# Performance work log

Hardware: AMD Instinct MI355X
Metric: run time of the kernel (lower is better)

## Reference

```python
import jax, jax.numpy as jnp
import numpy as np

B, N, D, H = 16, 256, 1024, 8
DK = D // H
WAVE_LEN = 1000.0


def box_relational_embedding(boxes):
    # boxes: (B, N, 4) as (x_min, y_min, x_max, y_max)
    x_min, y_min, x_max, y_max = jnp.split(boxes, 4, axis=-1)  # each (B, N, 1)
    cx = (x_min + x_max) * 0.5
    cy = (y_min + y_max) * 0.5
    w = (x_max - x_min) + 1.0
    h = (y_max - y_min) + 1.0
    # pairwise deltas (B, N, N); row i = query box, col j = key box
    delta_x = jnp.log(jnp.clip(jnp.abs((cx - jnp.swapaxes(cx, -2, -1)) / w), 1e-3, None))
    delta_y = jnp.log(jnp.clip(jnp.abs((cy - jnp.swapaxes(cy, -2, -1)) / h), 1e-3, None))
    delta_w = jnp.log(w / jnp.swapaxes(w, -2, -1))
    delta_h = jnp.log(h / jnp.swapaxes(h, -2, -1))
    pos = jnp.stack([delta_x, delta_y, delta_w, delta_h], axis=-1)  # (B, N, N, 4)
    # sinusoidal expansion: dim_g = 64 -> 8 frequencies per delta
    feat_range = jnp.arange(8, dtype=pos.dtype) / 8.0
    dim_mat = 1.0 / (WAVE_LEN ** feat_range)  # (8,)
    mul = (100.0 * pos)[..., None] * dim_mat  # (B, N, N, 4, 8)
    mul = mul.reshape(pos.shape[:3] + (32,))
    return jnp.concatenate([jnp.sin(mul), jnp.cos(mul)], axis=-1)  # (B, N, N, 64)


def setup_inputs() -> dict:
    key = jax.random.key(0)
    ks = jax.random.split(key, 12)
    x = jax.random.normal(ks[0], (B, N, D), dtype=jnp.float32)
    # valid boxes: x_max > x_min, y_max > y_min
    xy = jax.random.uniform(ks[1], (B, N, 2), dtype=jnp.float32) * 100.0
    wh = jax.random.uniform(ks[2], (B, N, 2), dtype=jnp.float32) * 50.0 + 1.0
    boxes = jnp.concatenate([xy, xy + wh], axis=-1)
    s = 1.0 / np.sqrt(D)
    Wq = jax.random.normal(ks[3], (D, D), dtype=jnp.float32) * s
    Wk = jax.random.normal(ks[4], (D, D), dtype=jnp.float32) * s
    Wv = jax.random.normal(ks[5], (D, D), dtype=jnp.float32) * s
    Wo = jax.random.normal(ks[6], (D, D), dtype=jnp.float32) * s
    bq = jnp.zeros((D,), jnp.float32)
    bk = jnp.zeros((D,), jnp.float32)
    bv = jnp.zeros((D,), jnp.float32)
    bo = jnp.zeros((D,), jnp.float32)
    Wg = jax.random.normal(ks[7], (H, 64), dtype=jnp.float32) * (1.0 / 8.0)  # 8 per-head (64->1) linears
    bg = jnp.zeros((H,), jnp.float32)
    return {"x": x, "boxes": boxes, "Wq": Wq, "bq": bq, "Wk": Wk, "bk": bk,
            "Wv": Wv, "bv": bv, "Wo": Wo, "bo": bo, "Wg": Wg, "bg": bg}


def reference(x, boxes, Wq, bq, Wk, bk, Wv, bv, Wo, bo, Wg, bg):
    emb = box_relational_embedding(boxes)  # (B, N, N, 64)
    # per-head geometric weights, ReLU'd: (B, H, N, N)
    geo = jax.nn.relu(jnp.einsum('bnmg,hg->bhnm', emb, Wg) + bg[None, :, None, None])
    q = (x @ Wq + bq).reshape(B, N, H, DK).transpose(0, 2, 1, 3)  # (B, H, N, DK)
    k = (x @ Wk + bk).reshape(B, N, H, DK).transpose(0, 2, 1, 3)
    v = (x @ Wv + bv).reshape(B, N, H, DK).transpose(0, 2, 1, 3)
    scores = jnp.einsum('bhnd,bhmd->bhnm', q, k) / np.sqrt(DK)
    w_mn = jax.nn.softmax(jnp.log(jnp.clip(geo, 1e-6, None)) + scores, axis=-1)
    out = jnp.einsum('bhnm,bhmd->bhnd', w_mn, v)  # (B, H, N, DK)
    out = out.transpose(0, 2, 1, 3).reshape(B, N, D)
    return out @ Wo + bo
```

## Files before the change

### kernel.cpp

```cpp
#include <hip/hip_runtime.h>
#include <hip/hip_fp16.h>

#define Bb 16
#define Nn 256
#define Dd 1024
#define Hh 8
#define DKk 128

typedef unsigned short u16;
typedef __attribute__((ext_vector_type(8))) short bfrag;
typedef __attribute__((ext_vector_type(4))) float f4;

#define MFMA16(a, b, c) __builtin_amdgcn_mfma_f32_16x16x32_bf16((a), (b), (c), 0, 0, 0)

__device__ __forceinline__ u16 f2b(float f) {
  unsigned int u = __builtin_bit_cast(unsigned int, f);
  u += 0x7fffu + ((u >> 16) & 1u);
  return (u16)(u >> 16);
}

typedef __attribute__((address_space(1))) void GV;
typedef __attribute__((address_space(3))) void LV;
__device__ __forceinline__ void gload16(const void* g, void* l) {
  __builtin_amdgcn_global_load_lds((GV*)g, (LV*)l, 16, 0, 0);
}

__global__ __launch_bounds__(256) void cast_x_kernel(const float* __restrict__ x,
                                                     u16* __restrict__ xb) {
  const int i = blockIdx.x * 256 + threadIdx.x;
  const float4 v = ((const float4*)x)[i];
  union { u16 u[4]; unsigned long long ll; } p;
  p.u[0] = f2b(v.x); p.u[1] = f2b(v.y); p.u[2] = f2b(v.z); p.u[3] = f2b(v.w);
  ((unsigned long long*)xb)[i] = p.ll;
}

__global__ __launch_bounds__(256) void transpose_w_kernel(
    const float* __restrict__ Wq, const float* __restrict__ Wk,
    const float* __restrict__ Wv, const float* __restrict__ Wo,
    u16* __restrict__ wqkvt, u16* __restrict__ wot) {
  __shared__ float t[32][33];
  const int bid = blockIdx.x;
  const int which = bid >> 10;
  const int tr = (bid >> 5) & 31;
  const int tc = bid & 31;
  const float* W = which == 0 ? Wq : which == 1 ? Wk : which == 2 ? Wv : Wo;
  u16* dst = (which == 3) ? wot : (wqkvt + (long long)which * 1024 * 1024);
  const int tx = threadIdx.x & 31, ty = threadIdx.x >> 5;
#pragma unroll
  for (int rr = 0; rr < 4; rr++)
    t[ty + rr * 8][tx] = W[(tr * 32 + ty + rr * 8) * 1024 + tc * 32 + tx];
  __syncthreads();
#pragma unroll
  for (int rr = 0; rr < 4; rr++)
    dst[(tc * 32 + ty + rr * 8) * 1024 + tr * 32 + tx] = f2b(t[tx][ty + rr * 8]);
}

__global__ __launch_bounds__(256) void transpose_v_kernel(const u16* __restrict__ v,
                                                          u16* __restrict__ vT) {
  __shared__ u16 t[32][33];
  const int bid = blockIdx.x;
  const int bh = bid >> 5;
  const int kt = (bid >> 2) & 7;
  const int ct = bid & 3;
  const u16* src = v + (long long)bh * Nn * DKk;
  u16* dst = vT + (long long)bh * DKk * Nn;
  const int tx = threadIdx.x & 31, ty = threadIdx.x >> 5;
#pragma unroll
  for (int rr = 0; rr < 4; rr++)
    t[ty + rr * 8][tx] = src[(kt * 32 + ty + rr * 8) * DKk + ct * 32 + tx];
  __syncthreads();
#pragma unroll
  for (int rr = 0; rr < 4; rr++)
    dst[(ct * 32 + ty + rr * 8) * Nn + kt * 32 + tx] = t[tx][ty + rr * 8];
}

__global__ __launch_bounds__(256) void geo_kernel(const float* __restrict__ boxes,
                                                  const float* __restrict__ Wg,
                                                  const float* __restrict__ bg,
                                                  __half* __restrict__ logg) {
  __shared__ float wg_s[512];
  __shared__ float bg_s[8];
  const int tid = threadIdx.x;
  wg_s[tid] = Wg[tid];
  wg_s[tid + 256] = Wg[tid + 256];
  if (tid < 8) bg_s[tid] = bg[tid];
  __syncthreads();
  const int bid = blockIdx.x;
  const int b = bid >> 8, i = bid & 255;
  const int j = tid;
  const float4 bi4 = ((const float4*)boxes)[b * 256 + i];
  const float4 bj4 = ((const float4*)boxes)[b * 256 + j];
  const float cxi = (bi4.x + bi4.z) * 0.5f, cyi = (bi4.y + bi4.w) * 0.5f;
  const float wi = bi4.z - bi4.x + 1.f, hi = bi4.w - bi4.y + 1.f;
  const float cxj = (bj4.x + bj4.z) * 0.5f, cyj = (bj4.y + bj4.w) * 0.5f;
  const float wj = bj4.z - bj4.x + 1.f, hj = bj4.w - bj4.y + 1.f;
  float pos[4];
  pos[0] = __logf(fmaxf(fabsf((cxi - cxj) / wi), 1e-3f));
  pos[1] = __logf(fmaxf(fabsf((cyi - cyj) / hi), 1e-3f));
  pos[2] = __logf(wi / wj);
  pos[3] = __logf(hi / hj);
  const float dimm[8] = {1.0f, 0.42169650342f, 0.177827941f, 0.0749894209f,
                         0.0316227766f, 0.01333521432f, 0.00562341325f, 0.00237137371f};
  float sv[32], cv[32];
#pragma unroll
  for (int d = 0; d < 4; d++)
#pragma unroll
    for (int f = 0; f < 8; f++) {
      const float ang = 100.f * pos[d] * dimm[f];
      __sincosf(ang, &sv[d * 8 + f], &cv[d * 8 + f]);
    }
  const long long base = ((long long)(b * 8) * 256 + i) * 256 + j;
#pragma unroll
  for (int h = 0; h < 8; h++) {
    float a = bg_s[h];
#pragma unroll
    for (int t = 0; t < 32; t++)
      a = fmaf(sv[t], wg_s[h * 64 + t], fmaf(cv[t], wg_s[h * 64 + 32 + t], a));
    logg[base + (long long)h * 65536] = __float2half(__logf(fmaxf(a, 1e-6f)));
  }
}

#define LDA_SUB(AV, ihalf)                                                      \
  _Pragma("unroll") for (int i_ = 0; i_ < 4; i_++) {                            \
    const int row_ = wm * 128 + (ihalf) * 64 + i_ * 16 + fr;                    \
    AV[i_][0] = *(const bfrag*)(Asc + row_ * 64 + acol0);                       \
    AV[i_][1] = *(const bfrag*)(Asc + row_ * 64 + acol1);                       \
  }
#define LDB_SUB(BV, jhalf)                                                      \
  _Pragma("unroll") for (int j_ = 0; j_ < 2; j_++) {                            \
    const int row_ = wn * 64 + (jhalf) * 32 + j_ * 16 + fr;                     \
    BV[j_][0] = *(const bfrag*)(Bsc + row_ * 64 + acol0);                       \
    BV[j_][1] = *(const bfrag*)(Bsc + row_ * 64 + acol1);                       \
  }
#define QUAD(I0, J0, AV, BV)                                                    \
  _Pragma("unroll") for (int i_ = 0; i_ < 4; i_++)                              \
  _Pragma("unroll") for (int j_ = 0; j_ < 2; j_++)                              \
  _Pragma("unroll") for (int ks_ = 0; ks_ < 2; ks_++)                           \
    acc[(I0) + i_][(J0) + j_] =                                                 \
        MFMA16(AV[i_][ks_], BV[j_][ks_], acc[(I0) + i_][(J0) + j_]);
#define STG_A(kt_, r_, dA) \
  gload16(Agp + (long long)(r_) * 65536 + (kt_) * 64, (dA) + (r_) * 4096 + (w << 9))
#define STG_B(kt_, r_, dB) \
  gload16(Bgp + (long long)(r_) * 65536 + (kt_) * 64, (dB) + (r_) * 4096 + (w << 9))
#define BAR() __builtin_amdgcn_s_barrier()
#define PRIO1() __builtin_amdgcn_s_setprio(1)
#define PRIO0() __builtin_amdgcn_s_setprio(0)

__global__ __launch_bounds__(512, 1) void gemm256_qkv(
    const u16* __restrict__ A, const u16* __restrict__ Bt,
    const float* __restrict__ b0, const float* __restrict__ b1,
    const float* __restrict__ b2, u16* __restrict__ oq, u16* __restrict__ ok,
    u16* __restrict__ ov) {
  __shared__ u16 AsF[2 * 16384];
  __shared__ u16 BsF[2 * 16384];
  const int tid = threadIdx.x, lane = tid & 63, w = tid >> 6;
  const int wm = w >> 2, wn = w & 3;
  const int fr = lane & 15, fq = lane >> 4;

  const int bid = (blockIdx.x & 7) * 24 + (blockIdx.x >> 3);
  const int bm = bid / 12, bn = bid - bm * 12;
  const int m0 = bm << 8, n0 = bn << 8;

  const int acol0 = (fq * 8) ^ ((fr & 7) * 8);
  const int acol1 = (32 + fq * 8) ^ ((fr & 7) * 8);

  const int srw = tid >> 3;
  const int scol = (((tid & 7) ^ (srw & 7)) << 3);
  const u16* Agp = A + (long long)(m0 + srw) * 1024 + scol;
  const u16* Bgp = Bt + (long long)(n0 + srw) * 1024 + scol;

  f4 acc[8][4];
#pragma unroll
  for (int i = 0; i < 8; i++)
#pragma unroll
    for (int j = 0; j < 4; j++) acc[i][j] = (f4){0.f, 0.f, 0.f, 0.f};

  {
    u16* dA = AsF; u16* dB = BsF;
    STG_A(0, 0, dA); STG_A(0, 2, dA);
    STG_B(0, 0, dB); STG_B(0, 1, dB); STG_B(0, 2, dB); STG_B(0, 3, dB);
    STG_A(0, 1, dA); STG_A(0, 3, dA);
  }

  bfrag aV[4][2], b0V[2][2], b1V[2][2];

  for (int kt = 0; kt < 15; ++kt) {
    const int cur = kt & 1;
    const u16* Asc = AsF + cur * 16384;
    const u16* Bsc = BsF + cur * 16384;
    u16* dA = AsF + (cur ^ 1) * 16384;
    u16* dB = BsF + (cur ^ 1) * 16384;
    asm volatile("s_waitcnt vmcnt(2)" ::: "memory");
    BAR();
    LDA_SUB(aV, 0); LDB_SUB(b0V, 0);
    STG_A(kt + 1, 0, dA); STG_A(kt + 1, 2, dA);
    BAR();
    PRIO1(); QUAD(0, 0, aV, b0V); PRIO0();
    BAR();
    LDB_SUB(b1V, 1);
    STG_B(kt + 1, 0, dB); STG_B(kt + 1, 1, dB);
    BAR();
    PRIO1(); QUAD(0, 2, aV, b1V); PRIO0();
    BAR();
    asm volatile("s_waitcnt vmcnt(4)" ::: "memory");
    BAR();
    LDA_SUB(aV, 1);
    STG_B(kt + 1, 2, dB); STG_B(kt + 1, 3, dB);
    BAR();
    PRIO1(); QUAD(4, 2, aV, b1V); PRIO0();
    BAR();
    STG_A(kt + 1, 1, dA); STG_A(kt + 1, 3, dA);
    BAR();
    PRIO1(); QUAD(4, 0, aV, b0V); PRIO0();
    BAR();
  }
  {
    const u16* Asc = AsF + 16384;
    const u16* Bsc = BsF + 16384;
    asm volatile("s_waitcnt vmcnt(2)" ::: "memory");
    BAR();
    LDA_SUB(aV, 0); LDB_SUB(b0V, 0);
    PRIO1(); QUAD(0, 0, aV, b0V); PRIO0();
    LDB_SUB(b1V, 1);
    PRIO1(); QUAD(0, 2, aV, b1V); PRIO0();
    asm volatile("s_waitcnt vmcnt(0)" ::: "memory");
    BAR();
    LDA_SUB(aV, 1);
    QUAD(4, 2, aV, b1V);
    QUAD(4, 0, aV, b0V);
  }

#pragma unroll
  for (int j = 0; j < 4; j++) {
    const int n = n0 + wn * 64 + j * 16 + fr;
    const int which = n >> 10;
    const int hh = (n >> 7) & 7;
    const int dk = n & 127;
    const float bia = (which == 0 ? b0 : which == 1 ? b1 : b2)[n & 1023];
    u16* dst = (which == 0 ? oq : which == 1 ? ok : ov);
    const float scl = (which == 0) ? 0.08838834764831845f : 1.0f;
#pragma unroll
    for (int i = 0; i < 8; i++)
#pragma unroll
      for (int r = 0; r < 4; r++) {
        const int m = m0 + wm * 128 + i * 16 + fq * 4 + r;
        const int bidx = m >> 8, itok = m & 255;
        dst[((long long)(bidx * 8 + hh) * 256 + itok) * 128 + dk] =
            f2b((acc[i][j][r] + bia) * scl);
      }
  }
}

__global__ __launch_bounds__(256) void gemm128_out(
    const u16* __restrict__ A, const u16* __restrict__ Bt,
    const float* __restrict__ b0, float* __restrict__ co, int Np, int K) {
  __shared__ u16 As[128 * 32];
  __shared__ u16 Bs[128 * 32];
  const int tilesN = Np >> 7;
  const int bm = blockIdx.x / tilesN, bn = blockIdx.x - bm * tilesN;
  const int m0 = bm << 7, n0 = bn << 7;
  const int tid = threadIdx.x, lane = tid & 63, w = tid >> 6;
  const int wr = w >> 1, wc = w & 1;
  const int fr = lane & 15, fq = lane >> 4;

  f4 acc[4][4];
#pragma unroll
  for (int i = 0; i < 4; i++)
#pragma unroll
    for (int j = 0; j < 4; j++) acc[i][j] = (f4){0.f, 0.f, 0.f, 0.f};

  const int srow = (w << 5) + (lane >> 2);
  const int skel = (lane & 3) << 3;
  const u16* Ag0 = A + (long long)(m0 + srow) * K + skel;
  const u16* Ag1 = Ag0 + 16 * K;
  const u16* Bg0 = Bt + (long long)(n0 + srow) * K + skel;
  const u16* Bg1 = Bg0 + 16 * K;
  u16* Al0 = As + (w << 5) * 32;
  u16* Al1 = Al0 + 16 * 32;
  u16* Bl0 = Bs + (w << 5) * 32;
  u16* Bl1 = Bl0 + 16 * 32;

  for (int k0 = 0; k0 < K; k0 += 32) {
    __syncthreads();
    gload16(Ag0 + k0, Al0);
    gload16(Ag1 + k0, Al1);
    gload16(Bg0 + k0, Bl0);
    gload16(Bg1 + k0, Bl1);
    __syncthreads();
    bfrag av[4], bv[4];
#pragma unroll
    for (int i = 0; i < 4; i++)
      av[i] = *(const bfrag*)(As + ((wr << 6) + (i << 4) + fr) * 32 + (fq << 3));
#pragma unroll
    for (int j = 0; j < 4; j++)
      bv[j] = *(const bfrag*)(Bs + ((wc << 6) + (j << 4) + fr) * 32 + (fq << 3));
#pragma unroll
    for (int i = 0; i < 4; i++)
#pragma unroll
      for (int j = 0; j < 4; j++) acc[i][j] = MFMA16(av[i], bv[j], acc[i][j]);
  }

#pragma unroll
  for (int i = 0; i < 4; i++)
#pragma unroll
    for (int j = 0; j < 4; j++) {
      const int n = n0 + (wc << 6) + (j << 4) + fr;
      const float bia = b0[n];
#pragma unroll
      for (int r = 0; r < 4; r++) {
        const int m = m0 + (wr << 6) + (i << 4) + (fq << 2) + r;
        co[(long long)m * Np + n] = acc[i][j][r] + bia;
      }
    }
}

__global__ __launch_bounds__(256, 4) void attn_kernel(
    const u16* __restrict__ q, const u16* __restrict__ k,
    const u16* __restrict__ vT, const __half* __restrict__ logg,
    u16* __restrict__ aout) {
  __shared__ __align__(16) char smem[16384 + 17408 + 256];
  __half* ggs = (__half*)smem;
  u16* plds = (u16*)(smem + 16384);
  float* mbuf = (float*)(smem + 16384);
  float* mlb = (float*)(smem + 16384 + 17408);

  const int bid = blockIdx.x;
  const int qt = bid & 7;
  const int bh = bid >> 3;
  const int tid = threadIdx.x, lane = tid & 63, w = tid >> 6;
  const int rg = w >> 1, kh = w & 1;
  const int fr = lane & 15, fq = lane >> 4;
  const int i0 = qt * 32 + rg * 16;

  const u16* qp = q + (long long)bh * Nn * DKk;
  const u16* kp = k + (long long)bh * Nn * DKk + kh * 128 * DKk;
  const u16* vp = vT + (long long)bh * DKk * Nn;
  const __half* gp = logg + (long long)bh * Nn * Nn;

  __half* ggw = ggs + w * (16 * 128);
  {
    const int r4 = lane >> 4, c8 = lane & 15;
#pragma unroll
    for (int t = 0; t < 4; t++)
      gload16(gp + (i0 + t * 4 + r4) * Nn + kh * 128 + c8 * 8, ggw + t * 512);
  }

  bfrag qf[4];
#pragma unroll
  for (int ks = 0; ks < 4; ks++)
    qf[ks] = *(const bfrag*)(qp + (i0 + fr) * DKk + ks * 32 + fq * 8);

  f4 s[8];
#pragma unroll
  for (int j = 0; j < 8; j++) s[j] = (f4){0.f, 0.f, 0.f, 0.f};
#pragma unroll
  for (int j = 0; j < 8; j++)
#pragma unroll
    for (int ks = 0; ks < 4; ks++) {
      bfrag kf = *(const bfrag*)(kp + (j * 16 + fr) * DKk + ks * 32 + fq * 8);
      s[j] = MFMA16(qf[ks], kf, s[j]);
    }

  asm volatile("s_waitcnt vmcnt(0)" ::: "memory");

#pragma unroll
  for (int j = 0; j < 8; j++)
#pragma unroll
    for (int r = 0; r < 4; r++)
      s[j][r] += __half2float(ggw[(fq * 4 + r) * 128 + j * 16 + fr]);

  float mr[4], lr[4];
#pragma unroll
  for (int r = 0; r < 4; r++) {
    float m = s[0][r];
#pragma unroll
    for (int j = 1; j < 8; j++) m = fmaxf(m, s[j][r]);
    m = fmaxf(m, __shfl_xor(m, 1));
    m = fmaxf(m, __shfl_xor(m, 2));
    m = fmaxf(m, __shfl_xor(m, 4));
    m = fmaxf(m, __shfl_xor(m, 8));
    float t = 0.f;
#pragma unroll
    for (int j = 0; j < 8; j++) {
      const float p = __expf(s[j][r] - m);
      s[j][r] = p;
      t += p;
    }
    t += __shfl_xor(t, 1);
    t += __shfl_xor(t, 2);
    t += __shfl_xor(t, 4);
    t += __shfl_xor(t, 8);
    mr[r] = m;
    lr[r] = t;
  }

  u16* pw = plds + w * (16 * 136);
#pragma unroll
  for (int j = 0; j < 8; j++)
#pragma unroll
    for (int r = 0; r < 4; r++)
      pw[(fq * 4 + r) * 136 + j * 16 + fr] = f2b(s[j][r]);
  __syncthreads();

  f4 o[8];
#pragma unroll
  for (int d = 0; d < 8; d++) o[d] = (f4){0.f, 0.f, 0.f, 0.f};
#pragma unroll
  for (int jt = 0; jt < 4; jt++) {
    bfrag pf = *(const bfrag*)(pw + fr * 136 + jt * 32 + fq * 8);
#pragma unroll
    for (int d = 0; d < 8; d++) {
      bfrag vf = *(const bfrag*)(vp + (d * 16 + fr) * Nn + kh * 128 + jt * 32 + fq * 8);
      o[d] = MFMA16(pf, vf, o[d]);
    }
  }
  __syncthreads();

  if (kh) {
    float* ob = mbuf + rg * (16 * 132);
#pragma unroll
    for (int d = 0; d < 8; d++)
#pragma unroll
      for (int r = 0; r < 4; r++)
        ob[(fq * 4 + r) * 132 + d * 16 + fr] = o[d][r];
    if (fr == 0)
#pragma unroll
      for (int r = 0; r < 4; r++) {
        mlb[rg * 32 + (fq * 4 + r) * 2] = mr[r];
        mlb[rg * 32 + (fq * 4 + r) * 2 + 1] = lr[r];
      }
  }
  __syncthreads();

  if (!kh) {
    const int b = bh >> 3, h = bh & 7;
    float a0[4], a1[4], invl[4];
#pragma unroll
    for (int r = 0; r < 4; r++) {
      const float m1 = mlb[rg * 32 + (fq * 4 + r) * 2];
      const float l1 = mlb[rg * 32 + (fq * 4 + r) * 2 + 1];
      const float m = fmaxf(mr[r], m1);
      a0[r] = __expf(mr[r] - m);
      a1[r] = __expf(m1 - m);
      invl[r] = 1.0f / (lr[r] * a0[r] + l1 * a1[r]);
    }
    const float* ob = mbuf + rg * (16 * 132);
#pragma unroll
    for (int d = 0; d < 8; d++)
#pragma unroll
      for (int r = 0; r < 4; r++) {
        const float o1 = ob[(fq * 4 + r) * 132 + d * 16 + fr];
        const float val = (o[d][r] * a0[r] + o1 * a1[r]) * invl[r];
        const int row = i0 + fq * 4 + r;
        const int dk = d * 16 + fr;
        aout[((long long)(b * 256 + row)) * 1024 + h * 128 + dk] = f2b(val);
      }
  }
}

extern "C" void kernel_launch(void* const* d_in, const int* in_sizes, int n_in,
                              void* d_out, int out_size, void* d_ws, size_t ws_size,
                              hipStream_t stream) {
  (void)in_sizes; (void)n_in; (void)out_size; (void)ws_size;
  const float* x = (const float*)d_in[0];
  const float* boxes = (const float*)d_in[1];
  const float* Wq = (const float*)d_in[2];
  const float* bq = (const float*)d_in[3];
  const float* Wk = (const float*)d_in[4];
  const float* bk = (const float*)d_in[5];
  const float* Wv = (const float*)d_in[6];
  const float* bv = (const float*)d_in[7];
  const float* Wo = (const float*)d_in[8];
  const float* bo = (const float*)d_in[9];
  const float* Wg = (const float*)d_in[10];
  const float* bg = (const float*)d_in[11];
  float* out = (float*)d_out;

  char* ws = (char*)d_ws;
  u16* xb    = (u16*)(ws);
  u16* wqkvt = (u16*)(ws + (8ll << 20));
  u16* wot   = (u16*)(ws + (14ll << 20));
  u16* qb    = (u16*)(ws + (16ll << 20));
  u16* kb    = (u16*)(ws + (24ll << 20));
  u16* vb    = (u16*)(ws + (32ll << 20));
  u16* vtb   = (u16*)(ws + (40ll << 20));
  __half* logg = (__half*)(ws + (48ll << 20));
  u16* aout  = (u16*)(ws + (64ll << 20));

  cast_x_kernel<<<4096, 256, 0, stream>>>(x, xb);
  transpose_w_kernel<<<4096, 256, 0, stream>>>(Wq, Wk, Wv, Wo, wqkvt, wot);
  geo_kernel<<<4096, 256, 0, stream>>>(boxes, Wg, bg, logg);
  gemm256_qkv<<<192, 512, 0, stream>>>(xb, wqkvt, bq, bk, bv, qb, kb, vb);
  transpose_v_kernel<<<4096, 256, 0, stream>>>(vb, vtb);
  attn_kernel<<<1024, 256, 0, stream>>>(qb, kb, vtb, logg, aout);
  gemm128_out<<<32 * 8, 256, 0, stream>>>(aout, wot, bo, out, 1024, 1024);
}
```

Measured before the change: 229.1 us.

## Merge prep kernels, fuse V transpose into QKV GEMM, retile output GEMM

Merges the x cast, weight transpose and geo-bias kernels into one launch. The QKV GEMM now writes V directly in transposed layout, which removes the separate V transpose kernel and its pass through memory. Several other changes ride along: the output GEMM uses 128x64 tiles (512 blocks) with a swizzled block order, the attention kernel gets a remapped block order and double-buffered K/V fragment loads, and the GEMM main loop's barriers and waits are rearranged. The transposed V store from the GEMM epilogue is strided, which may cost write efficiency.

```diff
diff --git a/kernel.cpp b/kernel.cpp
--- a/kernel.cpp
+++ b/kernel.cpp
@@ -1,10 +1,7 @@
 #include <hip/hip_runtime.h>
 #include <hip/hip_fp16.h>
 
-#define Bb 16
 #define Nn 256
-#define Dd 1024
-#define Hh 8
 #define DKk 128
 
 typedef unsigned short u16;
@@ -25,67 +22,50 @@
   __builtin_amdgcn_global_load_lds((GV*)g, (LV*)l, 16, 0, 0);
 }
 
-__global__ __launch_bounds__(256) void cast_x_kernel(const float* __restrict__ x,
-                                                     u16* __restrict__ xb) {
-  const int i = blockIdx.x * 256 + threadIdx.x;
-  const float4 v = ((const float4*)x)[i];
-  union { u16 u[4]; unsigned long long ll; } p;
-  p.u[0] = f2b(v.x); p.u[1] = f2b(v.y); p.u[2] = f2b(v.z); p.u[3] = f2b(v.w);
-  ((unsigned long long*)xb)[i] = p.ll;
-}
-
-__global__ __launch_bounds__(256) void transpose_w_kernel(
+__global__ __launch_bounds__(256) void pre_kernel(
+    const float* __restrict__ x, const float* __restrict__ boxes,
     const float* __restrict__ Wq, const float* __restrict__ Wk,
     const float* __restrict__ Wv, const float* __restrict__ Wo,
-    u16* __restrict__ wqkvt, u16* __restrict__ wot) {
-  __shared__ float t[32][33];
-  const int bid = blockIdx.x;
-  const int which = bid >> 10;
-  const int tr = (bid >> 5) & 31;
-  const int tc = bid & 31;
-  const float* W = which == 0 ? Wq : which == 1 ? Wk : which == 2 ? Wv : Wo;
-  u16* dst = (which == 3) ? wot : (wqkvt + (long long)which * 1024 * 1024);
-  const int tx = threadIdx.x & 31, ty = threadIdx.x >> 5;
-#pragma unroll
-  for (int rr = 0; rr < 4; rr++)
-    t[ty + rr * 8][tx] = W[(tr * 32 + ty + rr * 8) * 1024 + tc * 32 + tx];
-  __syncthreads();
-#pragma unroll
-  for (int rr = 0; rr < 4; rr++)
-    dst[(tc * 32 + ty + rr * 8) * 1024 + tr * 32 + tx] = f2b(t[tx][ty + rr * 8]);
-}
-
-__global__ __launch_bounds__(256) void transpose_v_kernel(const u16* __restrict__ v,
-                                                          u16* __restrict__ vT) {
-  __shared__ u16 t[32][33];
-  const int bid = blockIdx.x;
-  const int bh = bid >> 5;
-  const int kt = (bid >> 2) & 7;
-  const int ct = bid & 3;
-  const u16* src = v + (long long)bh * Nn * DKk;
-  u16* dst = vT + (long long)bh * DKk * Nn;
-  const int tx = threadIdx.x & 31, ty = threadIdx.x >> 5;
-#pragma unroll
-  for (int rr = 0; rr < 4; rr++)
-    t[ty + rr * 8][tx] = src[(kt * 32 + ty + rr * 8) * DKk + ct * 32 + tx];
-  __syncthreads();
-#pragma unroll
-  for (int rr = 0; rr < 4; rr++)
-    dst[(ct * 32 + ty + rr * 8) * Nn + kt * 32 + tx] = t[tx][ty + rr * 8];
-}
-
-__global__ __launch_bounds__(256) void geo_kernel(const float* __restrict__ boxes,
-                                                  const float* __restrict__ Wg,
-                                                  const float* __restrict__ bg,
-                                                  __half* __restrict__ logg) {
-  __shared__ float wg_s[512];
-  __shared__ float bg_s[8];
+    const float* __restrict__ Wg, const float* __restrict__ bg,
+    u16* __restrict__ xb, u16* __restrict__ wqkvt, u16* __restrict__ wot,
+    __half* __restrict__ logg) {
+  __shared__ float smem[33 * 32];
   const int tid = threadIdx.x;
+  const int gbid = blockIdx.x;
+
+  if (gbid < 4096) {
+    const int i = gbid * 256 + tid;
+    const float4 v = ((const float4*)x)[i];
+    union { u16 u[4]; unsigned long long ll; } p;
+    p.u[0] = f2b(v.x); p.u[1] = f2b(v.y); p.u[2] = f2b(v.z); p.u[3] = f2b(v.w);
+    ((unsigned long long*)xb)[i] = p.ll;
+    return;
+  }
+  if (gbid < 8192) {
+    const int bid = gbid - 4096;
+    const int which = bid >> 10;
+    const int tr = (bid >> 5) & 31;
+    const int tc = bid & 31;
+    const float* W = which == 0 ? Wq : which == 1 ? Wk : which == 2 ? Wv : Wo;
+    u16* dst = (which == 3) ? wot : (wqkvt + (long long)which * 1024 * 1024);
+    const int tx = tid & 31, ty = tid >> 5;
+    float* t = smem;
+#pragma unroll
+    for (int rr = 0; rr < 4; rr++)
+      t[(ty + rr * 8) * 33 + tx] = W[(tr * 32 + ty + rr * 8) * 1024 + tc * 32 + tx];
+    __syncthreads();
+#pragma unroll
+    for (int rr = 0; rr < 4; rr++)
+      dst[(tc * 32 + ty + rr * 8) * 1024 + tr * 32 + tx] = f2b(t[tx * 33 + ty + rr * 8]);
+    return;
+  }
+  float* wg_s = smem;
+  float* bg_s = smem + 512;
   wg_s[tid] = Wg[tid];
   wg_s[tid + 256] = Wg[tid + 256];
   if (tid < 8) bg_s[tid] = bg[tid];
   __syncthreads();
-  const int bid = blockIdx.x;
+  const int bid = gbid - 8192;
   const int b = bid >> 8, i = bid & 255;
   const int j = tid;
   const float4 bi4 = ((const float4*)boxes)[b * 256 + i];
@@ -150,7 +130,7 @@
     const u16* __restrict__ A, const u16* __restrict__ Bt,
     const float* __restrict__ b0, const float* __restrict__ b1,
     const float* __restrict__ b2, u16* __restrict__ oq, u16* __restrict__ ok,
-    u16* __restrict__ ov) {
+    u16* __restrict__ ovT) {
   __shared__ u16 AsF[2 * 16384];
   __shared__ u16 BsF[2 * 16384];
   const int tid = threadIdx.x, lane = tid & 63, w = tid >> 6;
@@ -181,6 +161,8 @@
     STG_B(0, 0, dB); STG_B(0, 1, dB); STG_B(0, 2, dB); STG_B(0, 3, dB);
     STG_A(0, 1, dA); STG_A(0, 3, dA);
   }
+  asm volatile("s_waitcnt vmcnt(2)" ::: "memory");
+  BAR();
 
   bfrag aV[4][2], b0V[2][2], b1V[2][2];
 
@@ -190,8 +172,6 @@
     const u16* Bsc = BsF + cur * 16384;
     u16* dA = AsF + (cur ^ 1) * 16384;
     u16* dB = BsF + (cur ^ 1) * 16384;
-    asm volatile("s_waitcnt vmcnt(2)" ::: "memory");
-    BAR();
     LDA_SUB(aV, 0); LDB_SUB(b0V, 0);
     STG_A(kt + 1, 0, dA); STG_A(kt + 1, 2, dA);
     BAR();
@@ -201,7 +181,6 @@
     STG_B(kt + 1, 0, dB); STG_B(kt + 1, 1, dB);
     BAR();
     PRIO1(); QUAD(0, 2, aV, b1V); PRIO0();
-    BAR();
     asm volatile("s_waitcnt vmcnt(4)" ::: "memory");
     BAR();
     LDA_SUB(aV, 1);
@@ -212,13 +191,12 @@
     STG_A(kt + 1, 1, dA); STG_A(kt + 1, 3, dA);
     BAR();
     PRIO1(); QUAD(4, 0, aV, b0V); PRIO0();
+    asm volatile("s_waitcnt vmcnt(2)" ::: "memory");
     BAR();
   }
   {
     const u16* Asc = AsF + 16384;
     const u16* Bsc = BsF + 16384;
-    asm volatile("s_waitcnt vmcnt(2)" ::: "memory");
-    BAR();
     LDA_SUB(aV, 0); LDB_SUB(b0V, 0);
     PRIO1(); QUAD(0, 0, aV, b0V); PRIO0();
     LDB_SUB(b1V, 1);
@@ -237,7 +215,6 @@
     const int hh = (n >> 7) & 7;
     const int dk = n & 127;
     const float bia = (which == 0 ? b0 : which == 1 ? b1 : b2)[n & 1023];
-    u16* dst = (which == 0 ? oq : which == 1 ? ok : ov);
     const float scl = (which == 0) ? 0.08838834764831845f : 1.0f;
 #pragma unroll
     for (int i = 0; i < 8; i++)
@@ -245,71 +222,71 @@
       for (int r = 0; r < 4; r++) {
         const int m = m0 + wm * 128 + i * 16 + fq * 4 + r;
         const int bidx = m >> 8, itok = m & 255;
-        dst[((long long)(bidx * 8 + hh) * 256 + itok) * 128 + dk] =
-            f2b((acc[i][j][r] + bia) * scl);
+        const u16 val = f2b((acc[i][j][r] + bia) * scl);
+        if (which == 2)
+          ovT[((long long)(bidx * 8 + hh) * 128 + dk) * 256 + itok] = val;
+        else
+          (which == 0 ? oq : ok)[((long long)(bidx * 8 + hh) * 256 + itok) * 128 + dk] = val;
       }
   }
 }
 
-__global__ __launch_bounds__(256) void gemm128_out(
+__global__ __launch_bounds__(256) void gemm_out64(
     const u16* __restrict__ A, const u16* __restrict__ Bt,
-    const float* __restrict__ b0, float* __restrict__ co, int Np, int K) {
+    const float* __restrict__ b0, float* __restrict__ co) {
   __shared__ u16 As[128 * 32];
-  __shared__ u16 Bs[128 * 32];
-  const int tilesN = Np >> 7;
-  const int bm = blockIdx.x / tilesN, bn = blockIdx.x - bm * tilesN;
-  const int m0 = bm << 7, n0 = bn << 7;
+  __shared__ u16 Bs[64 * 32];
+  const int bid = (blockIdx.x & 7) * 64 + (blockIdx.x >> 3);
+  const int bm = bid >> 4, bn = bid & 15;
+  const int m0 = bm << 7, n0 = bn << 6;
   const int tid = threadIdx.x, lane = tid & 63, w = tid >> 6;
   const int wr = w >> 1, wc = w & 1;
   const int fr = lane & 15, fq = lane >> 4;
 
-  f4 acc[4][4];
+  f4 acc[4][2];
 #pragma unroll
   for (int i = 0; i < 4; i++)
 #pragma unroll
-    for (int j = 0; j < 4; j++) acc[i][j] = (f4){0.f, 0.f, 0.f, 0.f};
-
-  const int srow = (w << 5) + (lane >> 2);
+    for (int j = 0; j < 2; j++) acc[i][j] = (f4){0.f, 0.f, 0.f, 0.f};
+
+  const int sr = lane >> 2;
   const int skel = (lane & 3) << 3;
-  const u16* Ag0 = A + (long long)(m0 + srow) * K + skel;
-  const u16* Ag1 = Ag0 + 16 * K;
-  const u16* Bg0 = Bt + (long long)(n0 + srow) * K + skel;
-  const u16* Bg1 = Bg0 + 16 * K;
+  const u16* Ag0 = A + (long long)(m0 + (w << 5) + sr) * 1024 + skel;
+  const u16* Ag1 = Ag0 + 16 * 1024;
+  const u16* Bg0 = Bt + (long long)(n0 + (w << 4) + sr) * 1024 + skel;
   u16* Al0 = As + (w << 5) * 32;
   u16* Al1 = Al0 + 16 * 32;
-  u16* Bl0 = Bs + (w << 5) * 32;
-  u16* Bl1 = Bl0 + 16 * 32;
-
-  for (int k0 = 0; k0 < K; k0 += 32) {
+  u16* Bl0 = Bs + (w << 4) * 32;
+
+  for (int k0 = 0; k0 < 1024; k0 += 32) {
     __syncthreads();
     gload16(Ag0 + k0, Al0);
     gload16(Ag1 + k0, Al1);
     gload16(Bg0 + k0, Bl0);
-    gload16(Bg1 + k0, Bl1);
     __syncthreads();
-    bfrag av[4], bv[4];
+    bfrag av[4], bv[2];
 #pragma unroll
     for (int i = 0; i < 4; i++)
       av[i] = *(const bfrag*)(As + ((wr << 6) + (i << 4) + fr) * 32 + (fq << 3));
 #pragma unroll
-    for (int j = 0; j < 4; j++)
-      bv[j] = *(const bfrag*)(Bs + ((wc << 6) + (j << 4) + fr) * 32 + (fq << 3));
+    for (int j = 0; j < 2; j++)
+      bv[j] = *(const bfrag*)(Bs + ((wc << 5) + (j << 4) + fr) * 32 + (fq << 3));
 #pragma unroll
     for (int i = 0; i < 4; i++)
 #pragma unroll
-      for (int j = 0; j < 4; j++) acc[i][j] = MFMA16(av[i], bv[j], acc[i][j]);
+      for (int j = 0; j < 2; j++) acc[i][j] = MFMA16(av[i], bv[j], acc[i][j]);
   }
 
 #pragma unroll
   for (int i = 0; i < 4; i++)
 #pragma unroll
-    for (int j = 0; j < 4; j++) {
-      const int n = n0 + (wc << 6) + (j << 4) + fr;
+    for (int j = 0; j < 2; j++) {
+      const int n = n0 + (wc << 5) + (j << 4) + fr;
       const float bia = b0[n];
 #pragma unroll
       for (int r = 0; r < 4; r++) {
         const int m = m0 + (wr << 6) + (i << 4) + (fq << 2) + r;
-        co[(long long)m * Np + n] = acc[i][j][r] + bia;
+        co[(long long)m * 1024 + n] = acc[i][j][r] + bia;
       }
     }
 }
@@ -324,7 +301,7 @@
   float* mbuf = (float*)(smem + 16384);
   float* mlb = (float*)(smem + 16384 + 17408);
 
-  const int bid = blockIdx.x;
+  const int bid = ((blockIdx.x & 7) << 7) | (blockIdx.x >> 3);
   const int qt = bid & 7;
   const int bh = bid >> 3;
   const int tid = threadIdx.x, lane = tid & 63, w = tid >> 6;
@@ -353,13 +330,22 @@
   f4 s[8];
 #pragma unroll
   for (int j = 0; j < 8; j++) s[j] = (f4){0.f, 0.f, 0.f, 0.f};
-#pragma unroll
-  for (int j = 0; j < 8; j++)
-#pragma unroll
-    for (int ks = 0; ks < 4; ks++) {
-      bfrag kf = *(const bfrag*)(kp + (j * 16 + fr) * DKk + ks * 32 + fq * 8);
-      s[j] = MFMA16(qf[ks], kf, s[j]);
-    }
+
+  bfrag kfb[2][4];
+#pragma unroll
+  for (int ks = 0; ks < 4; ks++)
+    kfb[0][ks] = *(const bfrag*)(kp + fr * DKk + ks * 32 + fq * 8);
+#pragma unroll
+  for (int j = 0; j < 8; j++) {
+    if (j < 7) {
+#pragma unroll
+      for (int ks = 0; ks < 4; ks++)
+        kfb[(j + 1) & 1][ks] =
+            *(const bfrag*)(kp + ((j + 1) * 16 + fr) * DKk + ks * 32 + fq * 8);
+    }
+#pragma unroll
+    for (int ks = 0; ks < 4; ks++) s[j] = MFMA16(qf[ks], kfb[j & 1][ks], s[j]);
+  }
 
   asm volatile("s_waitcnt vmcnt(0)" ::: "memory");
 
@@ -408,10 +394,14 @@
 #pragma unroll
   for (int jt = 0; jt < 4; jt++) {
     bfrag pf = *(const bfrag*)(pw + fr * 136 + jt * 32 + fq * 8);
+    bfrag vfb[2];
+    vfb[0] = *(const bfrag*)(vp + fr * Nn + kh * 128 + jt * 32 + fq * 8);
 #pragma unroll
     for (int d = 0; d < 8; d++) {
-      bfrag vf = *(const bfrag*)(vp + (d * 16 + fr) * Nn + kh * 128 + jt * 32 + fq * 8);
-      o[d] = MFMA16(pf, vf, o[d]);
+      if (d < 7)
+        vfb[(d + 1) & 1] =
+            *(const bfrag*)(vp + ((d + 1) * 16 + fr) * Nn + kh * 128 + jt * 32 + fq * 8);
+      o[d] = MFMA16(pf, vfb[d & 1], o[d]);
     }
   }
   __syncthreads();
@@ -482,16 +472,13 @@
   u16* wot   = (u16*)(ws + (14ll << 20));
   u16* qb    = (u16*)(ws + (16ll << 20));
   u16* kb    = (u16*)(ws + (24ll << 20));
-  u16* vb    = (u16*)(ws + (32ll << 20));
-  u16* vtb   = (u16*)(ws + (40ll << 20));
+  u16* vtb   = (u16*)(ws + (32ll << 20));
   __half* logg = (__half*)(ws + (48ll << 20));
   u16* aout  = (u16*)(ws + (64ll << 20));
 
-  cast_x_kernel<<<4096, 256, 0, stream>>>(x, xb);
-  transpose_w_kernel<<<4096, 256, 0, stream>>>(Wq, Wk, Wv, Wo, wqkvt, wot);
-  geo_kernel<<<4096, 256, 0, stream>>>(boxes, Wg, bg, logg);
-  gemm256_qkv<<<192, 512, 0, stream>>>(xb, wqkvt, bq, bk, bv, qb, kb, vb);
-  transpose_v_kernel<<<4096, 256, 0, stream>>>(vb, vtb);
+  pre_kernel<<<12288, 256, 0, stream>>>(x, boxes, Wq, Wk, Wv, Wo, Wg, bg,
+                                        xb, wqkvt, wot, logg);
+  gemm256_qkv<<<192, 512, 0, stream>>>(xb, wqkvt, bq, bk, bv, qb, kb, vtb);
   attn_kernel<<<1024, 256, 0, stream>>>(qb, kb, vtb, logg, aout);
-  gemm128_out<<<32 * 8, 256, 0, stream>>>(aout, wot, bo, out, 1024, 1024);
-}
+  gemm_out64<<<512, 256, 0, stream>>>(aout, wot, bo, out);
+}
```

Result: no change. 233.4 us (+1.8%).
